# Kernel optimization log

Measured on AMD Instinct MI355X. Metric: run time of the kernel, lower is better.

The kernel has to match this reference:

```python
import jax, jax.numpy as jnp
import numpy as np

N_NODES = 100000
N_EDGES = 1600000
IN_FEATS = 128
NUM_HEADS = 4
OUT_FEATS = 32
NUM_ETYPES = 8
DROP_BLOCKS = 4


def setup_inputs() -> dict:
    key = jax.random.key(0)
    k1, k2, k3, k4, k5 = jax.random.split(key, 5)
    feat = jax.random.normal(k1, (N_NODES, IN_FEATS), dtype=jnp.float32)
    e_feat = jax.random.randint(k2, (N_EDGES,), 0, NUM_ETYPES, dtype=jnp.int32)
    src = jax.random.randint(k3, (N_EDGES,), 0, N_NODES, dtype=jnp.int32)
    dst = jax.random.randint(k4, (N_EDGES,), 0, N_NODES, dtype=jnp.int32)
    kf, ke = jax.random.split(k5)
    # xavier_normal with relu gain for fc: std = gain * sqrt(2/(fan_in+fan_out))
    gain = float(np.sqrt(2.0))
    std = gain * float(np.sqrt(2.0 / (IN_FEATS + NUM_HEADS * OUT_FEATS)))
    fc_weight = jax.random.normal(kf, (NUM_HEADS * OUT_FEATS, IN_FEATS), dtype=jnp.float32) * std
    # edge_emb initialized with normal_()
    edge_emb = jax.random.normal(ke, (NUM_ETYPES, NUM_HEADS), dtype=jnp.float32)
    return {"feat": feat, "fc_weight": fc_weight, "edge_emb": edge_emb,
            "e_feat": e_feat, "src": src, "dst": dst, "drop_blocks": DROP_BLOCKS}


def _edge_softmax(e, dst, n_nodes):
    # segmented softmax over incoming edges per destination node, per head
    # e: (E, H)
    m = jax.ops.segment_max(e, dst, num_segments=n_nodes)      # (N, H)
    z = jnp.exp(e - m[dst])                                    # (E, H)
    s = jax.ops.segment_sum(z, dst, num_segments=n_nodes)      # (N, H)
    return z / s[dst]


def reference(feat, fc_weight, edge_emb, e_feat, src, dst, drop_blocks):
    n = feat.shape[0]
    H = edge_emb.shape[1]
    D = fc_weight.shape[0] // H
    # fc projection -> (N, H, D); feat_drop is identity (p=0 / eval)
    ft = (feat @ fc_weight.T).reshape(n, H, D)
    # edge type embedding logits (E, H)
    ee = edge_emb[e_feat]
    attn = _edge_softmax(ee, dst, n)                           # (E, H)
    # mcdropedge with attn_drop p=0: attn broadcast over blocks is identity scaling
    # u_mul_e + sum: gather src features, scale by attn, scatter-sum into dst
    msg = ft[src] * attn[:, :, None]                           # (E, H, D)
    rst = jax.ops.segment_sum(msg, dst, num_segments=n)        # (N, H, D)
    # attn returned with mcdropedge expansion shape (E, H, drop_blocks, 1)
    attn_out = jnp.broadcast_to(attn[:, :, None], (attn.shape[0], H, drop_blocks))[..., None]
    return rst, attn_out
```

## Files before the change

### kernel.cpp

```cpp
#include <hip/hip_runtime.h>


typedef short short8 __attribute__((ext_vector_type(8)));
typedef unsigned short ushort8 __attribute__((ext_vector_type(8)));
typedef float f32x4 __attribute__((ext_vector_type(4)));

__device__ inline unsigned short f2bf(float x) {
    unsigned u = __builtin_bit_cast(unsigned, x);
    u += 0x7FFFu + ((u >> 16) & 1u);
    return (unsigned short)(u >> 16);
}

__global__ __launch_bounds__(256) void k_bcnt(const int* __restrict__ dst,
                                              unsigned* __restrict__ gcnt, int E) {
    __shared__ unsigned l[256];
    int tid = threadIdx.x;
    l[tid] = 0;
    __syncthreads();
    int base = blockIdx.x * 2048;
#pragma unroll
    for (int j = 0; j < 8; ++j) {
        int e = base + j * 256 + tid;
        if (e < E) atomicAdd(&l[(unsigned)dst[e] >> 9], 1u);
    }
    __syncthreads();
    if (l[tid]) atomicAdd(&gcnt[tid], l[tid]);
}

__global__ __launch_bounds__(256) void k_bscan(const unsigned* __restrict__ gcnt,
                                               unsigned* __restrict__ gbase,
                                               unsigned* __restrict__ gcur) {
    __shared__ unsigned s[256];
    int t = threadIdx.x;
    unsigned orig = gcnt[t];
    s[t] = orig;
    __syncthreads();
    for (int of = 1; of < 256; of <<= 1) {
        unsigned v = (t >= of) ? s[t - of] : 0u;
        __syncthreads();
        s[t] += v;
        __syncthreads();
    }
    unsigned eb = s[t] - orig;
    gbase[t] = eb;
    gcur[t] = eb;
}

__global__ __launch_bounds__(256) void k_part(const int* __restrict__ src,
                                              const int* __restrict__ dst,
                                              const int* __restrict__ ef,
                                              unsigned* __restrict__ gcur,
                                              unsigned* __restrict__ csr2,
                                              int E, int nbuk) {
    __shared__ unsigned lcnt[256];
    __shared__ unsigned lbase[256];
    __shared__ unsigned lcur[256];
    __shared__ unsigned gw2[256];
    __shared__ unsigned stp[4096];
    __shared__ unsigned short stb[4096];
    int tid = threadIdx.x;
    lcnt[tid] = 0;
    __syncthreads();

    int cb = blockIdx.x * 4096;
    int cc = E - cb; if (cc > 4096) cc = 4096;

    unsigned pay[16];
    unsigned short bk[16];
#pragma unroll
    for (int j = 0; j < 16; ++j) {
        int idx = j * 256 + tid;
        if (idx < cc) {
            int e = cb + idx;
            unsigned d = (unsigned)dst[e];
            pay[j] = (unsigned)src[e] | ((unsigned)ef[e] << 17) | ((d & 511u) << 20);
            bk[j] = (unsigned short)(d >> 9);
            atomicAdd(&lcnt[bk[j]], 1u);
        }
    }
    __syncthreads();
    lbase[tid] = lcnt[tid];
    __syncthreads();
    for (int of = 1; of < 256; of <<= 1) {
        unsigned v = (tid >= of) ? lbase[tid - of] : 0u;
        __syncthreads();
        lbase[tid] += v;
        __syncthreads();
    }
    unsigned eb = lbase[tid] - lcnt[tid];
    __syncthreads();
    lbase[tid] = eb;
    lcur[tid] = eb;
    __syncthreads();
#pragma unroll
    for (int j = 0; j < 16; ++j) {
        int idx = j * 256 + tid;
        if (idx < cc) {
            unsigned lpos = atomicAdd(&lcur[bk[j]], 1u);
            stp[lpos] = pay[j];
            stb[lpos] = bk[j];
        }
    }
    if (tid < nbuk && lcnt[tid]) gw2[tid] = atomicAdd(&gcur[tid], lcnt[tid]);
    __syncthreads();
#pragma unroll
    for (int j = 0; j < 16; ++j) {
        int i = j * 256 + tid;
        if (i < cc) {
            unsigned b = stb[i];
            csr2[gw2[b] + (i - lbase[b])] = stp[i];
        }
    }
}

__global__ __launch_bounds__(256) void k_bsort2(const unsigned* __restrict__ csr2,
                                                const unsigned* __restrict__ gbase,
                                                const unsigned* __restrict__ gcnt,
                                                const float* __restrict__ emb,
                                                unsigned* __restrict__ csr,
                                                unsigned* __restrict__ offs,
                                                unsigned* __restrict__ deg,
                                                float* __restrict__ stats, int N) {
    __shared__ unsigned cnt8[512 * 8];
    __shared__ unsigned degL[512];
    __shared__ unsigned offsL[512];
    __shared__ unsigned curL[512];
    __shared__ unsigned tmp[256];
    __shared__ float se[32];
    int b = blockIdx.x, tid = threadIdx.x;
    if (tid < 32) se[tid] = emb[tid];
#pragma unroll
    for (int i = 0; i < 16; ++i) cnt8[i * 256 + tid] = 0u;
    __syncthreads();
    unsigned r0 = gbase[b], r1 = r0 + gcnt[b];
    for (unsigned i = r0 + tid; i < r1; i += 256) {
        unsigned en = csr2[i];
        atomicAdd(&cnt8[((en >> 20) & 511u) * 8u + ((en >> 17) & 7u)], 1u);
    }
    __syncthreads();
    int n0 = tid * 2, n1 = tid * 2 + 1;
    unsigned d0 = 0, d1 = 0;
#pragma unroll
    for (int k = 0; k < 8; ++k) { d0 += cnt8[n0 * 8 + k]; d1 += cnt8[n1 * 8 + k]; }
    degL[n0] = d0; degL[n1] = d1;
    tmp[tid] = d0 + d1;
    __syncthreads();
    for (int of = 1; of < 256; of <<= 1) {
        unsigned v = (tid >= of) ? tmp[tid - of] : 0u;
        __syncthreads();
        tmp[tid] += v;
        __syncthreads();
    }
    unsigned eb = tmp[tid] - (d0 + d1);
    offsL[n0] = eb;        curL[n0] = eb;
    offsL[n1] = eb + d0;   curL[n1] = eb + d0;
#pragma unroll
    for (int q = 0; q < 2; ++q) {
        int nl = tid * 2 + q;
        int gn = b * 512 + nl;
        if (gn < N) {
            offs[gn] = r0 + offsL[nl];
            unsigned dg = degL[nl];
            deg[gn] = dg;
            const unsigned* c = &cnt8[nl * 8];
#pragma unroll
            for (int h = 0; h < 4; ++h) {
                float m = -3.4e38f;
#pragma unroll
                for (int tt = 0; tt < 8; ++tt)
                    if (c[tt]) m = fmaxf(m, se[tt * 4 + h]);
                float s = 0.f;
#pragma unroll
                for (int tt = 0; tt < 8; ++tt)
                    if (c[tt]) s += (float)c[tt] * expf(se[tt * 4 + h] - m);
                stats[(size_t)gn * 8 + h] = m;
                stats[(size_t)gn * 8 + 4 + h] = dg ? (1.0f / s) : 0.0f;
            }
        }
    }
    __syncthreads();
    for (unsigned i = r0 + tid; i < r1; i += 256) {
        unsigned en = csr2[i];
        unsigned nlo = (en >> 20) & 511u;
        unsigned tt = (en >> 17) & 7u;
        unsigned pos = r0 + atomicAdd(&curL[nlo], 1u);
        csr[pos] = (en & 0x1FFFFu) | (tt << 20);
    }
}

__global__ __launch_bounds__(256) void k_attn_out(const int* __restrict__ e_feat,
                                                  const int* __restrict__ dst,
                                                  const float* __restrict__ emb,
                                                  const float* __restrict__ stats,
                                                  float4* __restrict__ ao, int E) {
    int e = blockIdx.x * 256 + threadIdx.x;
    if (e >= E) return;
    int tt = e_feat[e];
    int d = dst[e];
    const float4* st4 = (const float4*)(stats + (size_t)d * 8);
    float4 m4 = st4[0], i4 = st4[1];
    float4 ee = *(const float4*)(emb + tt * 4);
    float a0 = expf(ee.x - m4.x) * i4.x;
    float a1 = expf(ee.y - m4.y) * i4.y;
    float a2 = expf(ee.z - m4.z) * i4.z;
    float a3 = expf(ee.w - m4.w) * i4.w;
    float4* p = ao + (size_t)e * 4;
    p[0] = make_float4(a0, a0, a0, a0);
    p[1] = make_float4(a1, a1, a1, a1);
    p[2] = make_float4(a2, a2, a2, a2);
    p[3] = make_float4(a3, a3, a3, a3);
}

__global__ __launch_bounds__(256) void k_gemm_mfma(const float* __restrict__ feat,
                                                   const float* __restrict__ W,
                                                   unsigned short* __restrict__ ftb, int N) {
    __shared__ unsigned short Sb[128 * 136];
    int tid = threadIdx.x;
    int row0 = blockIdx.x * 128;

#pragma unroll
    for (int it = 0; it < 16; ++it) {
        int i = it * 1024 + tid * 4;
        int r = i >> 7, c = i & 127;
        unsigned swz = (unsigned)((r & 7) << 4);
        float4 w4 = *(const float4*)(W + i);
        ushort4 wb;
        wb.x = f2bf(w4.x); wb.y = f2bf(w4.y); wb.z = f2bf(w4.z); wb.w = f2bf(w4.w);
        *(ushort4*)((char*)Sb + (((unsigned)(r * 256 + c * 2)) ^ swz)) = wb;
    }
    __syncthreads();

    int wv = tid >> 6, lane = tid & 63;
    int rl = lane & 15;
    unsigned swz = (unsigned)((lane & 7) << 4);
    int kq = (lane >> 4) * 16;
    int ko = (lane >> 4) * 8;

    int ra0 = row0 + wv * 32 + rl;
    int ra1 = ra0 + 16;
    bool v0 = ra0 < N, v1 = ra1 < N;
    const float* ap0 = feat + (size_t)ra0 * 128 + ko;
    const float* ap1 = feat + (size_t)ra1 * 128 + ko;

    f32x4 acc[2][8];
#pragma unroll
    for (int rt = 0; rt < 2; ++rt)
#pragma unroll
        for (int jt = 0; jt < 8; ++jt)
            acc[rt][jt] = (f32x4){0.f, 0.f, 0.f, 0.f};

    const char* Bb = (const char*)Sb;
#pragma unroll
    for (int kk = 0; kk < 4; ++kk) {
        int kb = kk * 64 + kq;
        short8 a[2], bfr[8];
#pragma unroll
        for (int rt = 0; rt < 2; ++rt) {
            const float* ap = rt ? ap1 : ap0;
            bool v = rt ? v1 : v0;
            float4 lo = make_float4(0.f, 0.f, 0.f, 0.f), hi = lo;
            if (v) { lo = *(const float4*)(ap + kk * 32); hi = *(const float4*)(ap + kk * 32 + 4); }
            short8 t;
            t[0] = (short)f2bf(lo.x); t[1] = (short)f2bf(lo.y);
            t[2] = (short)f2bf(lo.z); t[3] = (short)f2bf(lo.w);
            t[4] = (short)f2bf(hi.x); t[5] = (short)f2bf(hi.y);
            t[6] = (short)f2bf(hi.z); t[7] = (short)f2bf(hi.w);
            a[rt] = t;
        }
#pragma unroll
        for (int jt = 0; jt < 8; ++jt)
            bfr[jt] = *(const short8*)(Bb + (((unsigned)((jt * 16 + rl) * 256 + kb)) ^ swz));
#pragma unroll
        for (int rt = 0; rt < 2; ++rt)
#pragma unroll
            for (int jt = 0; jt < 8; ++jt)
                acc[rt][jt] = __builtin_amdgcn_mfma_f32_16x16x32_bf16(a[rt], bfr[jt], acc[rt][jt], 0, 0, 0);
    }

    __syncthreads();
#pragma unroll
    for (int rt = 0; rt < 2; ++rt) {
        int rbase = wv * 32 + rt * 16 + ((lane >> 4) << 2);
#pragma unroll
        for (int jt = 0; jt < 8; ++jt) {
            int col = jt * 16 + rl;
#pragma unroll
            for (int rg = 0; rg < 4; ++rg)
                Sb[(rbase + rg) * 136 + col] = f2bf(acc[rt][jt][rg]);
        }
    }
    __syncthreads();
#pragma unroll
    for (int g = 0; g < 8; ++g) {
        int rloc = g * 16 + (tid >> 4);
        int cc = (tid & 15) * 8;
        int gr = row0 + rloc;
        if (gr < N) {
            ushort8 v = *(const ushort8*)(&Sb[rloc * 136 + cc]);
            *(ushort8*)(ftb + (size_t)gr * 128 + cc) = v;
        }
    }
}

__global__ __launch_bounds__(256) void k_agg(const unsigned* __restrict__ csr,
                                             const unsigned* __restrict__ offs,
                                             const unsigned* __restrict__ deg,
                                             const float* __restrict__ stats,
                                             const float* __restrict__ emb,
                                             const unsigned* __restrict__ ftu,
                                             float* __restrict__ rst, int N) {
    __shared__ float wl[4 * 32];
    int tid = threadIdx.x;
    int wv = tid >> 6, lane = tid & 63;
    int n = blockIdx.x * 4 + wv;
    n = __builtin_amdgcn_readfirstlane(n);
    if (n < N && lane < 32) {
        int tt = lane >> 2, hh = lane & 3;
        float m = stats[(size_t)n * 8 + hh];
        float is = stats[(size_t)n * 8 + 4 + hh];
        wl[wv * 32 + lane] = expf(emb[tt * 4 + hh] - m) * is;
    }
    __syncthreads();
    if (n >= N) return;
    unsigned o = offs[n], dg = deg[n];
    int h = lane >> 4;
    const float* wlh = wl + wv * 32 + h;
    float accx = 0.f, accy = 0.f;
    for (unsigned kb = 0; kb < dg; kb += 64) {
        unsigned rem = dg - kb; if (rem > 64) rem = 64;
        unsigned centry = 0;
        if (lane < (int)rem) centry = csr[o + kb + lane];
        unsigned j = 0;
        for (; j + 8 <= rem; j += 8) {
            unsigned f[8]; float a[8];
#pragma unroll
            for (int jj = 0; jj < 8; ++jj) {
                unsigned e = __shfl(centry, (int)(j + jj), 64);
                f[jj] = ftu[(size_t)(e & 0xFFFFFu) * 64 + lane];
                a[jj] = wlh[(e >> 20) * 4];
            }
#pragma unroll
            for (int jj = 0; jj < 8; ++jj) {
                accx = fmaf(a[jj], __builtin_bit_cast(float, f[jj] << 16), accx);
                accy = fmaf(a[jj], __builtin_bit_cast(float, f[jj] & 0xFFFF0000u), accy);
            }
        }
        for (; j < rem; ++j) {
            unsigned e = __shfl(centry, (int)j, 64);
            unsigned f0 = ftu[(size_t)(e & 0xFFFFFu) * 64 + lane];
            float a0 = wlh[(e >> 20) * 4];
            accx = fmaf(a0, __builtin_bit_cast(float, f0 << 16), accx);
            accy = fmaf(a0, __builtin_bit_cast(float, f0 & 0xFFFF0000u), accy);
        }
    }
    ((float2*)rst)[(size_t)n * 64 + lane] = make_float2(accx, accy);
}

extern "C" void kernel_launch(void* const* d_in, const int* in_sizes, int n_in,
                              void* d_out, int out_size, void* d_ws, size_t ws_size,
                              hipStream_t stream) {
    const float* feat = (const float*)d_in[0];
    const float* W = (const float*)d_in[1];
    const float* emb = (const float*)d_in[2];
    const int* e_feat = (const int*)d_in[3];
    const int* src = (const int*)d_in[4];
    const int* dst = (const int*)d_in[5];
    int N = in_sizes[0] / 128;
    int E = in_sizes[3];
    int nbuk = (N + 511) >> 9;

    char* ws = (char*)d_ws;
    size_t off = 0;
    auto alloc = [&](size_t bytes) {
        void* p = ws + off;
        off = (off + bytes + 255) & ~(size_t)255;
        return p;
    };
    unsigned short* ftb = (unsigned short*)alloc((size_t)N * 128 * 2);
    float* stats = (float*)alloc((size_t)N * 8 * 4);
    unsigned* deg = (unsigned*)alloc((size_t)N * 4);
    unsigned* offs = (unsigned*)alloc((size_t)N * 4);
    unsigned* csr = (unsigned*)alloc((size_t)E * 4);
    unsigned* csr2 = (unsigned*)alloc((size_t)E * 4);
    unsigned* gcnt = (unsigned*)alloc(256 * 4);
    unsigned* gbase = (unsigned*)alloc(256 * 4);
    unsigned* gcur = (unsigned*)alloc(256 * 4);

    float* rst = (float*)d_out;
    float4* ao = (float4*)((float*)d_out + (size_t)N * 128);

    hipMemsetAsync(gcnt, 0, 256 * 4, stream);

    k_bcnt<<<(E + 2047) / 2048, 256, 0, stream>>>(dst, gcnt, E);
    k_bscan<<<1, 256, 0, stream>>>(gcnt, gbase, gcur);
    k_part<<<(E + 4095) / 4096, 256, 0, stream>>>(src, dst, e_feat, gcur, csr2, E, nbuk);
    k_bsort2<<<nbuk, 256, 0, stream>>>(csr2, gbase, gcnt, emb, csr, offs, deg, stats, N);
    k_gemm_mfma<<<(N + 127) / 128, 256, 0, stream>>>(feat, W, ftb, N);
    k_attn_out<<<(E + 255) / 256, 256, 0, stream>>>(e_feat, dst, emb, stats, ao, E);
    k_agg<<<(N + 3) / 4, 256, 0, stream>>>(csr, offs, deg, stats, emb, (const unsigned*)ftb, rst, N);
}
```

Baseline: 201.0 us.

## Widen aggregation gathers, coalesce attn output stores, drop global atomics in bucket count

The aggregation kernel now has each lane load 16-byte chunks of a source row, with four edges handled in parallel across the wavefront, then reduces the partial sums with xor shuffles before non-temporal stores. The attention output kernel stages values through shared memory so each thread writes contiguous float4s with non-temporal stores. Bucket counting writes per-block partials instead of using global atomics and a memset, and the scan sums those partials. bsort2 now reads the bucket end from gcur after partitioning, and the launch order is changed.

```diff
diff --git a/kernel.cpp b/kernel.cpp
--- a/kernel.cpp
+++ b/kernel.cpp
@@ -11,29 +11,45 @@
     return (unsigned short)(u >> 16);
 }
 
+__device__ inline void nt_store4(float* p, float a, float b, float c, float d) {
+    f32x4 v = (f32x4){a, b, c, d};
+    __builtin_nontemporal_store(v, (f32x4*)p);
+}
+
 __global__ __launch_bounds__(256) void k_bcnt(const int* __restrict__ dst,
-                                              unsigned* __restrict__ gcnt, int E) {
+                                              unsigned* __restrict__ gpart, int E) {
     __shared__ unsigned l[256];
     int tid = threadIdx.x;
     l[tid] = 0;
     __syncthreads();
-    int base = blockIdx.x * 2048;
-#pragma unroll
-    for (int j = 0; j < 8; ++j) {
+    int base = blockIdx.x * 4096;
+#pragma unroll
+    for (int j = 0; j < 16; ++j) {
         int e = base + j * 256 + tid;
         if (e < E) atomicAdd(&l[(unsigned)dst[e] >> 9], 1u);
     }
     __syncthreads();
-    if (l[tid]) atomicAdd(&gcnt[tid], l[tid]);
-}
-
-__global__ __launch_bounds__(256) void k_bscan(const unsigned* __restrict__ gcnt,
+    gpart[blockIdx.x * 256 + tid] = l[tid];
+}
+
+__global__ __launch_bounds__(256) void k_bscan(const unsigned* __restrict__ gpart,
+                                               int nchunk,
                                                unsigned* __restrict__ gbase,
                                                unsigned* __restrict__ gcur) {
     __shared__ unsigned s[256];
     int t = threadIdx.x;
-    unsigned orig = gcnt[t];
-    s[t] = orig;
+    unsigned sum = 0;
+    int r = 0;
+    for (; r + 4 <= nchunk; r += 4) {
+        unsigned a0 = gpart[(r + 0) * 256 + t];
+        unsigned a1 = gpart[(r + 1) * 256 + t];
+        unsigned a2 = gpart[(r + 2) * 256 + t];
+        unsigned a3 = gpart[(r + 3) * 256 + t];
+        sum += a0 + a1 + a2 + a3;
+    }
+    for (; r < nchunk; ++r) sum += gpart[r * 256 + t];
+    unsigned orig = sum;
+    s[t] = sum;
     __syncthreads();
     for (int of = 1; of < 256; of <<= 1) {
         unsigned v = (t >= of) ? s[t - of] : 0u;
@@ -115,7 +131,7 @@
 
 __global__ __launch_bounds__(256) void k_bsort2(const unsigned* __restrict__ csr2,
                                                 const unsigned* __restrict__ gbase,
-                                                const unsigned* __restrict__ gcnt,
+                                                const unsigned* __restrict__ gend,
                                                 const float* __restrict__ emb,
                                                 unsigned* __restrict__ csr,
                                                 unsigned* __restrict__ offs,
@@ -132,7 +148,7 @@
 #pragma unroll
     for (int i = 0; i < 16; ++i) cnt8[i * 256 + tid] = 0u;
     __syncthreads();
-    unsigned r0 = gbase[b], r1 = r0 + gcnt[b];
+    unsigned r0 = gbase[b], r1 = gend[b];
     for (unsigned i = r0 + tid; i < r1; i += 256) {
         unsigned en = csr2[i];
         atomicAdd(&cnt8[((en >> 20) & 511u) * 8u + ((en >> 17) & 7u)], 1u);
@@ -192,23 +208,38 @@
                                                   const int* __restrict__ dst,
                                                   const float* __restrict__ emb,
                                                   const float* __restrict__ stats,
-                                                  float4* __restrict__ ao, int E) {
-    int e = blockIdx.x * 256 + threadIdx.x;
-    if (e >= E) return;
-    int tt = e_feat[e];
-    int d = dst[e];
-    const float4* st4 = (const float4*)(stats + (size_t)d * 8);
-    float4 m4 = st4[0], i4 = st4[1];
-    float4 ee = *(const float4*)(emb + tt * 4);
-    float a0 = expf(ee.x - m4.x) * i4.x;
-    float a1 = expf(ee.y - m4.y) * i4.y;
-    float a2 = expf(ee.z - m4.z) * i4.z;
-    float a3 = expf(ee.w - m4.w) * i4.w;
-    float4* p = ao + (size_t)e * 4;
-    p[0] = make_float4(a0, a0, a0, a0);
-    p[1] = make_float4(a1, a1, a1, a1);
-    p[2] = make_float4(a2, a2, a2, a2);
-    p[3] = make_float4(a3, a3, a3, a3);
+                                                  float* __restrict__ ao, int E) {
+    __shared__ float av[4 * 257];
+    int tid = threadIdx.x;
+    int e = blockIdx.x * 256 + tid;
+    float a0 = 0.f, a1 = 0.f, a2 = 0.f, a3 = 0.f;
+    if (e < E) {
+        int tt = e_feat[e];
+        int d = dst[e];
+        const float4* st4 = (const float4*)(stats + (size_t)d * 8);
+        float4 m4 = st4[0], i4 = st4[1];
+        float4 ee = *(const float4*)(emb + tt * 4);
+        a0 = expf(ee.x - m4.x) * i4.x;
+        a1 = expf(ee.y - m4.y) * i4.y;
+        a2 = expf(ee.z - m4.z) * i4.z;
+        a3 = expf(ee.w - m4.w) * i4.w;
+    }
+    av[0 * 257 + tid] = a0;
+    av[1 * 257 + tid] = a1;
+    av[2 * 257 + tid] = a2;
+    av[3 * 257 + tid] = a3;
+    __syncthreads();
+    size_t base = (size_t)blockIdx.x * 1024;
+    size_t lim = (size_t)E * 4;
+#pragma unroll
+    for (int r = 0; r < 4; ++r) {
+        size_t g = base + r * 256 + tid;
+        if (g < lim) {
+            int gl = r * 256 + tid;
+            float v = av[(gl & 3) * 257 + (gl >> 2)];
+            nt_store4(ao + g * 4, v, v, v, v);
+        }
+    }
 }
 
 __global__ __launch_bounds__(256) void k_gemm_mfma(const float* __restrict__ feat,
@@ -307,7 +338,7 @@
                                              const unsigned* __restrict__ deg,
                                              const float* __restrict__ stats,
                                              const float* __restrict__ emb,
-                                             const unsigned* __restrict__ ftu,
+                                             const uint4* __restrict__ ft4,
                                              float* __restrict__ rst, int N) {
     __shared__ float wl[4 * 32];
     int tid = threadIdx.x;
@@ -323,37 +354,65 @@
     __syncthreads();
     if (n >= N) return;
     unsigned o = offs[n], dg = deg[n];
-    int h = lane >> 4;
+    int cl = lane & 15;
+    int es = lane >> 4;
+    int h = cl >> 2;
     const float* wlh = wl + wv * 32 + h;
-    float accx = 0.f, accy = 0.f;
+    float acc[8];
+#pragma unroll
+    for (int i = 0; i < 8; ++i) acc[i] = 0.f;
+
     for (unsigned kb = 0; kb < dg; kb += 64) {
         unsigned rem = dg - kb; if (rem > 64) rem = 64;
         unsigned centry = 0;
         if (lane < (int)rem) centry = csr[o + kb + lane];
-        unsigned j = 0;
-        for (; j + 8 <= rem; j += 8) {
-            unsigned f[8]; float a[8];
-#pragma unroll
-            for (int jj = 0; jj < 8; ++jj) {
-                unsigned e = __shfl(centry, (int)(j + jj), 64);
-                f[jj] = ftu[(size_t)(e & 0xFFFFFu) * 64 + lane];
-                a[jj] = wlh[(e >> 20) * 4];
+        unsigned g = 0;
+        for (; g + 16 <= rem; g += 16) {
+            uint4 f[4]; float a[4];
+#pragma unroll
+            for (int q = 0; q < 4; ++q) {
+                unsigned e = __shfl(centry, (int)(g + q * 4 + es), 64);
+                f[q] = ft4[(size_t)(e & 0xFFFFFu) * 16 + cl];
+                a[q] = wlh[(e >> 20) * 4];
             }
 #pragma unroll
-            for (int jj = 0; jj < 8; ++jj) {
-                accx = fmaf(a[jj], __builtin_bit_cast(float, f[jj] << 16), accx);
-                accy = fmaf(a[jj], __builtin_bit_cast(float, f[jj] & 0xFFFF0000u), accy);
+            for (int q = 0; q < 4; ++q) {
+                acc[0] = fmaf(a[q], __builtin_bit_cast(float, f[q].x << 16), acc[0]);
+                acc[1] = fmaf(a[q], __builtin_bit_cast(float, f[q].x & 0xFFFF0000u), acc[1]);
+                acc[2] = fmaf(a[q], __builtin_bit_cast(float, f[q].y << 16), acc[2]);
+                acc[3] = fmaf(a[q], __builtin_bit_cast(float, f[q].y & 0xFFFF0000u), acc[3]);
+                acc[4] = fmaf(a[q], __builtin_bit_cast(float, f[q].z << 16), acc[4]);
+                acc[5] = fmaf(a[q], __builtin_bit_cast(float, f[q].z & 0xFFFF0000u), acc[5]);
+                acc[6] = fmaf(a[q], __builtin_bit_cast(float, f[q].w << 16), acc[6]);
+                acc[7] = fmaf(a[q], __builtin_bit_cast(float, f[q].w & 0xFFFF0000u), acc[7]);
             }
         }
-        for (; j < rem; ++j) {
-            unsigned e = __shfl(centry, (int)j, 64);
-            unsigned f0 = ftu[(size_t)(e & 0xFFFFFu) * 64 + lane];
-            float a0 = wlh[(e >> 20) * 4];
-            accx = fmaf(a0, __builtin_bit_cast(float, f0 << 16), accx);
-            accy = fmaf(a0, __builtin_bit_cast(float, f0 & 0xFFFF0000u), accy);
-        }
-    }
-    ((float2*)rst)[(size_t)n * 64 + lane] = make_float2(accx, accy);
+        for (; g < rem; g += 4) {
+            int eidx = (int)g + es;
+            bool valid = eidx < (int)rem;
+            unsigned e = __shfl(centry, valid ? eidx : (int)g, 64);
+            uint4 f = ft4[(size_t)(e & 0xFFFFFu) * 16 + cl];
+            float a = valid ? wlh[(e >> 20) * 4] : 0.f;
+            acc[0] = fmaf(a, __builtin_bit_cast(float, f.x << 16), acc[0]);
+            acc[1] = fmaf(a, __builtin_bit_cast(float, f.x & 0xFFFF0000u), acc[1]);
+            acc[2] = fmaf(a, __builtin_bit_cast(float, f.y << 16), acc[2]);
+            acc[3] = fmaf(a, __builtin_bit_cast(float, f.y & 0xFFFF0000u), acc[3]);
+            acc[4] = fmaf(a, __builtin_bit_cast(float, f.z << 16), acc[4]);
+            acc[5] = fmaf(a, __builtin_bit_cast(float, f.z & 0xFFFF0000u), acc[5]);
+            acc[6] = fmaf(a, __builtin_bit_cast(float, f.w << 16), acc[6]);
+            acc[7] = fmaf(a, __builtin_bit_cast(float, f.w & 0xFFFF0000u), acc[7]);
+        }
+    }
+#pragma unroll
+    for (int i = 0; i < 8; ++i) {
+        acc[i] += __shfl_xor(acc[i], 16, 64);
+        acc[i] += __shfl_xor(acc[i], 32, 64);
+    }
+    if (lane < 16) {
+        float* op = rst + (size_t)n * 128 + cl * 8;
+        nt_store4(op, acc[0], acc[1], acc[2], acc[3]);
+        nt_store4(op + 4, acc[4], acc[5], acc[6], acc[7]);
+    }
 }
 
 extern "C" void kernel_launch(void* const* d_in, const int* in_sizes, int n_in,
@@ -368,6 +427,7 @@
     int N = in_sizes[0] / 128;
     int E = in_sizes[3];
     int nbuk = (N + 511) >> 9;
+    int nchunk = (E + 4095) / 4096;
 
     char* ws = (char*)d_ws;
     size_t off = 0;
@@ -382,20 +442,18 @@
     unsigned* offs = (unsigned*)alloc((size_t)N * 4);
     unsigned* csr = (unsigned*)alloc((size_t)E * 4);
     unsigned* csr2 = (unsigned*)alloc((size_t)E * 4);
-    unsigned* gcnt = (unsigned*)alloc(256 * 4);
+    unsigned* gpart = (unsigned*)alloc((size_t)nchunk * 256 * 4);
     unsigned* gbase = (unsigned*)alloc(256 * 4);
     unsigned* gcur = (unsigned*)alloc(256 * 4);
 
     float* rst = (float*)d_out;
-    float4* ao = (float4*)((float*)d_out + (size_t)N * 128);
-
-    hipMemsetAsync(gcnt, 0, 256 * 4, stream);
-
-    k_bcnt<<<(E + 2047) / 2048, 256, 0, stream>>>(dst, gcnt, E);
-    k_bscan<<<1, 256, 0, stream>>>(gcnt, gbase, gcur);
-    k_part<<<(E + 4095) / 4096, 256, 0, stream>>>(src, dst, e_feat, gcur, csr2, E, nbuk);
-    k_bsort2<<<nbuk, 256, 0, stream>>>(csr2, gbase, gcnt, emb, csr, offs, deg, stats, N);
+    float* ao = (float*)d_out + (size_t)N * 128;
+
+    k_bcnt<<<nchunk, 256, 0, stream>>>(dst, gpart, E);
+    k_bscan<<<1, 256, 0, stream>>>(gpart, nchunk, gbase, gcur);
+    k_part<<<nchunk, 256, 0, stream>>>(src, dst, e_feat, gcur, csr2, E, nbuk);
+    k_bsort2<<<nbuk, 256, 0, stream>>>(csr2, gbase, gcur, emb, csr, offs, deg, stats, N);
+    k_attn_out<<<(E + 255) / 256, 256, 0, stream>>>(e_feat, dst, emb, stats, ao, E);
     k_gemm_mfma<<<(N + 127) / 128, 256, 0, stream>>>(feat, W, ftb, N);
-    k_attn_out<<<(E + 255) / 256, 256, 0, stream>>>(e_feat, dst, emb, stats, ao, E);
-    k_agg<<<(N + 3) / 4, 256, 0, stream>>>(csr, offs, deg, stats, emb, (const unsigned*)ftb, rst, N);
-}
+    k_agg<<<(N + 3) / 4, 256, 0, stream>>>(csr, offs, deg, stats, emb, (const uint4*)ftb, rst, N);
+}
```

Result: faster. 178.7 us (-11.1%).
